# Kernel tuning notes

Hardware: AMD Instinct MI355X
Metric: run time of the kernel (lower is better)

The kernel has to match this reference:

```python
import jax, jax.numpy as jnp
import numpy as np

EPS = 1e-5
RS = 2                 # trilinear sampling points per bin per dim (fixed sampling_ratio)
OUT_SIZE = (4, 7, 7)   # (T_out, H_out, W_out)


def hswish(x):
    return x * jnp.clip(x + 3.0, 0.0, 6.0) / 6.0


def bn3d(x, g, b, m, v):
    # eval-mode BatchNorm3d over channel dim 1 of [N,C,T,H,W]
    s = g * jax.lax.rsqrt(v + EPS)
    return x * s[None, :, None, None, None] + (b - m * s)[None, :, None, None, None]


def conv3d(x, w, stride=1, pad=0, groups=1):
    return jax.lax.conv_general_dilated(
        x, w, window_strides=(stride,) * 3, padding=[(pad, pad)] * 3,
        dimension_numbers=('NCDHW', 'OIDHW', 'NCDHW'), feature_group_count=groups)


def roi_align_3d(feat, start, end):
    # feat: [N,C,T,H,W]; start/end: [N,3] in (x, y, t) order (one ROI per sample)
    N, C, T, H, W = feat.shape
    Pt, Ph, Pw = OUT_SIZE

    def coords(s, e, P):
        size = jnp.maximum(e - s, 1.0)
        # flattened sample j = bin*RS + i -> position s + (j+0.5)/RS * bin_size
        offs = (jnp.arange(P * RS, dtype=feat.dtype) + 0.5) / RS
        return s[:, None] + offs[None, :] * (size / P)[:, None]  # [N, P*RS]

    cx = coords(start[:, 0], end[:, 0], Pw)
    cy = coords(start[:, 1], end[:, 1], Ph)
    ct = coords(start[:, 2], end[:, 2], Pt)

    def lin(v, c, L):
        # linear interpolation of v along its last axis at continuous coords c
        c = jnp.clip(c, 0.0, L - 1.0)
        lo = jnp.floor(c).astype(jnp.int32)
        hi = jnp.minimum(lo + 1, L - 1)
        w = c - lo.astype(c.dtype)
        return v[..., lo] * (1.0 - w) + v[..., hi] * w

    def one(f, tt, ty, tx):
        f = lin(f, tx, W)                   # [C,T,H,Sw]
        f = jnp.moveaxis(f, 2, -1)          # [C,T,Sw,H]
        f = lin(f, ty, H)                   # [C,T,Sw,Sh]
        f = jnp.moveaxis(f, 1, -1)          # [C,Sw,Sh,T]
        f = lin(f, tt, T)                   # [C,Sw,Sh,St]
        f = jnp.transpose(f, (0, 3, 2, 1))  # [C,St,Sh,Sw]
        f = f.reshape(f.shape[0], Pt, RS, Ph, RS, Pw, RS)
        return f.mean(axis=(2, 4, 6))       # average sample points per bin

    return jax.vmap(one)(feat, ct, cy, cx)  # [N,C,Pt,Ph,Pw]


def setup_inputs():
    key = jax.random.key(0)
    ks = jax.random.split(key, 9)
    N, Cin, T, H, W = 64, 256, 8, 16, 16
    Cr = 128

    def bn_params(k, c):
        k1, k2, k3, k4 = jax.random.split(k, 4)
        g = jax.random.uniform(k1, (c,), minval=0.5, maxval=1.5)
        b = 0.1 * jax.random.normal(k2, (c,))
        m = 0.1 * jax.random.normal(k3, (c,))
        v = jax.random.uniform(k4, (c,), minval=0.5, maxval=1.5)
        return g, b, m, v

    x = jax.random.normal(ks[0], (N, Cin, T, H, W), jnp.float32)
    w1 = jax.random.normal(ks[1], (Cr, Cin, 1, 1, 1)) / np.float32(np.sqrt(Cin))
    wdw = jax.random.normal(ks[2], (Cr, 1, 3, 3, 3)) / np.float32(np.sqrt(27))
    w2 = jax.random.normal(ks[3], (Cr, Cr, 1, 1, 1)) / np.float32(np.sqrt(Cr))
    w3 = jax.random.normal(ks[4], (6, Cr, 1, 1, 1)) / np.float32(np.sqrt(Cr))
    g1, b1, m1, v1 = bn_params(ks[5], Cr)
    g2, b2, m2, v2 = bn_params(ks[6], Cr)
    g3, b3, m3, v3 = bn_params(ks[7], Cr)
    g4, b4, m4, v4 = bn_params(ks[8], 6)
    return dict(x=x, w1=w1, g1=g1, b1=b1, m1=m1, v1=v1,
                wdw=wdw, g2=g2, b2=b2, m2=m2, v2=v2,
                w2=w2, g3=g3, b3=b3, m3=m3, v3=v3,
                w3=w3, g4=g4, b4=b4, m4=m4, v4=v4)


def reference(x, w1, g1, b1, m1, v1, wdw, g2, b2, m2, v2,
              w2, g3, b3, m3, v3, w3, g4, b4, m4, v4):
    N, C, T, H, W = x.shape
    h = hswish(bn3d(conv3d(x, w1), g1, b1, m1, v1))
    h = hswish(bn3d(conv3d(h, wdw, stride=2, pad=1, groups=wdw.shape[0]), g2, b2, m2, v2))
    h = hswish(bn3d(conv3d(h, w2), g3, b3, m3, v3))
    # AvgPool3d with kernel == reduced feature size -> global spatial-temporal mean
    h = jnp.mean(h, axis=(2, 3, 4), keepdims=True)
    logits = bn3d(conv3d(h, w3), g4, b4, m4, v4).reshape(N, 6)
    lim = jax.nn.sigmoid(logits)   # eval path (gumbel only in training)
    scales = jnp.array([W, H, T], dtype=x.dtype)      # (x, y, t) order
    start = 0.5 * lim[:, :3] * scales
    end = (1.0 - 0.5 * lim[:, 3:]) * scales
    return roi_align_3d(x, start, end)
```

## Files before the change

### kernel.cpp

```cpp
#include <hip/hip_runtime.h>
#include <math.h>

#define N_BATCH 64
#define CIN 256
#define CR 128
#define T_IN 8
#define H_IN 16
#define W_IN 16
#define S1 2048
#define T2 4
#define H2 8
#define W2 8
#define S2 256
#define PT 4
#define PH 7
#define PW 7
#define EPSB 1e-5f

typedef __attribute__((ext_vector_type(8))) short bf16x8;
typedef __attribute__((ext_vector_type(4))) float f32x4;
typedef __attribute__((ext_vector_type(4))) unsigned int u32x4;
typedef __attribute__((ext_vector_type(8))) unsigned short ushort8;

__device__ __forceinline__ float hswish(float y) {
    float c = fminf(fmaxf(y + 3.0f, 0.0f), 6.0f);
    return y * c * (1.0f / 6.0f);
}

__device__ __forceinline__ unsigned int fbits(float x) {
    return __float_as_uint(x);
}

__device__ __forceinline__ unsigned int pkbf16(float lo, float hi) {
    return ((fbits(lo) + 0x8000u) >> 16) | ((fbits(hi) + 0x8000u) & 0xFFFF0000u);
}

__global__ __launch_bounds__(256) void wsplit_kernel(
    const float* __restrict__ w1, unsigned short* __restrict__ whi,
    unsigned short* __restrict__ wlo, float* __restrict__ pp)
{
    int i = blockIdx.x * 256 + threadIdx.x;
    int co = i >> 8;
    int k  = i & 255;
    float x = w1[i];
    unsigned int bx = fbits(x);
    unsigned int h = (bx + 0x8000u) & 0xFFFF0000u;
    float r = x - __uint_as_float(h);
    int flat = ((((co >> 4) * 8 + (k >> 5)) * 4 + ((k >> 3) & 3)) * 16 + (co & 15)) * 8 + (k & 7);
    whi[flat] = (unsigned short)(h >> 16);
    wlo[flat] = (unsigned short)((fbits(r) + 0x8000u) >> 16);
    pp[i] = 0.0f;
}

#define BFIDX(g, h, e, ln) (((((g) * 2 + (h)) * 2 + (e)) * 16 + (ln)) * 4)

__global__ __launch_bounds__(256, 5) void conv1_mfma_kernel(
    const float* __restrict__ x,
    const unsigned short* __restrict__ whi, const unsigned short* __restrict__ wlo,
    const float* __restrict__ g, const float* __restrict__ b,
    const float* __restrict__ m, const float* __restrict__ v,
    unsigned short* __restrict__ h1b)
{
    __shared__ unsigned int Bf[2][1024];

    int blk = blockIdx.x;
    int n  = blk >> 5;
    int s0 = (blk & 31) << 6;
    int tid = threadIdx.x;
    int wave = tid >> 6;
    int lane = tid & 63;
    int gl   = lane >> 4;
    int ln16 = lane & 15;
    int hw   = wave & 1;
    int wcoG = (wave >> 1) * 4;

    int sg = tid >> 6;
    int sc = tid & 63;
    int sh = sc >> 5;
    int se = sc & 1;
    int sl = (sc & 31) >> 1;
    int wslot = BFIDX(sg, sh, se, sl);
    const float* xg = x + (size_t)n * CIN * S1 + s0 + sc;

    f32x4 acc[4][2];
    #pragma unroll
    for (int i = 0; i < 4; i++) {
        acc[i][0] = (f32x4){0.f, 0.f, 0.f, 0.f};
        acc[i][1] = (f32x4){0.f, 0.f, 0.f, 0.f};
    }

    {
        float val[8];
        #pragma unroll
        for (int j = 0; j < 8; j++)
            val[j] = xg[(size_t)(sg * 8 + j) * S1];
        u32x4 w;
        #pragma unroll
        for (int p = 0; p < 4; p++)
            w[p] = pkbf16(val[2 * p], val[2 * p + 1]);
        *reinterpret_cast<u32x4*>(&Bf[0][wslot]) = w;
    }
    __syncthreads();

    #pragma unroll
    for (int ks = 0; ks < 8; ks++) {
        float val[8];
        if (ks < 7) {
            #pragma unroll
            for (int j = 0; j < 8; j++)
                val[j] = xg[(size_t)((ks + 1) * 32 + sg * 8 + j) * S1];
        }
        union { u32x4 u; bf16x8 bv; } B0, B1;
        B0.u = *reinterpret_cast<const u32x4*>(&Bf[ks & 1][BFIDX(gl, hw, 0, ln16)]);
        B1.u = *reinterpret_cast<const u32x4*>(&Bf[ks & 1][BFIDX(gl, hw, 1, ln16)]);
        {
            bf16x8 Ah[4];
            #pragma unroll
            for (int fc = 0; fc < 4; fc++) {
                int off = ((((wcoG + fc) * 8 + ks) * 4 + gl) * 16 + ln16) * 8;
                Ah[fc] = *reinterpret_cast<const bf16x8*>(whi + off);
            }
            #pragma unroll
            for (int fc = 0; fc < 4; fc++) {
                acc[fc][0] = __builtin_amdgcn_mfma_f32_16x16x32_bf16(Ah[fc], B0.bv, acc[fc][0], 0, 0, 0);
                acc[fc][1] = __builtin_amdgcn_mfma_f32_16x16x32_bf16(Ah[fc], B1.bv, acc[fc][1], 0, 0, 0);
            }
        }
        {
            bf16x8 Al[4];
            #pragma unroll
            for (int fc = 0; fc < 4; fc++) {
                int off = ((((wcoG + fc) * 8 + ks) * 4 + gl) * 16 + ln16) * 8;
                Al[fc] = *reinterpret_cast<const bf16x8*>(wlo + off);
            }
            #pragma unroll
            for (int fc = 0; fc < 4; fc++) {
                acc[fc][0] = __builtin_amdgcn_mfma_f32_16x16x32_bf16(Al[fc], B0.bv, acc[fc][0], 0, 0, 0);
                acc[fc][1] = __builtin_amdgcn_mfma_f32_16x16x32_bf16(Al[fc], B1.bv, acc[fc][1], 0, 0, 0);
            }
        }
        if (ks < 7) {
            u32x4 w;
            #pragma unroll
            for (int p = 0; p < 4; p++)
                w[p] = pkbf16(val[2 * p], val[2 * p + 1]);
            *reinterpret_cast<u32x4*>(&Bf[(ks + 1) & 1][wslot]) = w;
            __syncthreads();
        }
    }

    #pragma unroll
    for (int fc = 0; fc < 4; fc++)
        #pragma unroll
        for (int reg = 0; reg < 4; reg++) {
            int co = (wcoG + fc) * 16 + gl * 4 + reg;
            float sc_ = g[co] * rsqrtf(v[co] + EPSB);
            float tt = fmaf(-m[co], sc_, b[co]);
            float y0 = hswish(fmaf(acc[fc][0][reg], sc_, tt));
            float y1 = hswish(fmaf(acc[fc][1][reg], sc_, tt));
            unsigned int pk = pkbf16(y0, y1);
            *reinterpret_cast<unsigned int*>(
                h1b + ((size_t)n * CR + co) * S1 + s0 + hw * 32 + ln16 * 2) = pk;
        }
}

__global__ __launch_bounds__(256) void dwconv_kernel(
    const unsigned short* __restrict__ h1b, const float* __restrict__ wdw,
    const float* __restrict__ g, const float* __restrict__ b,
    const float* __restrict__ m, const float* __restrict__ v,
    float* __restrict__ h2)
{
    __shared__ float s[T_IN][H_IN][W_IN];
    __shared__ float wl[27];
    int blk = blockIdx.x;
    int n = blk >> 7;
    int c = blk & 127;
    int tid = threadIdx.x;
    const unsigned short* in = h1b + ((size_t)n * CR + c) * S1;

    {
        int e = tid * 8;
        ushort8 u = *reinterpret_cast<const ushort8*>(in + e);
        float* sp = &s[0][0][0] + e;
        #pragma unroll
        for (int i = 0; i < 8; i++)
            sp[i] = __uint_as_float((unsigned int)(unsigned short)u[i] << 16);
    }
    if (tid < 27) wl[tid] = wdw[c * 27 + tid];
    __syncthreads();

    int wo = tid & 7;
    int ho = (tid >> 3) & 7;
    int to = tid >> 6;
    float acc = 0.0f;
    #pragma unroll
    for (int dt = 0; dt < 3; dt++) {
        int ti = 2 * to - 1 + dt;
        if (ti < 0 || ti >= T_IN) continue;
        #pragma unroll
        for (int dh = 0; dh < 3; dh++) {
            int hi = 2 * ho - 1 + dh;
            if (hi < 0 || hi >= H_IN) continue;
            #pragma unroll
            for (int dw = 0; dw < 3; dw++) {
                int wi = 2 * wo - 1 + dw;
                if (wi < 0 || wi >= W_IN) continue;
                acc = fmaf(wl[(dt * 3 + dh) * 3 + dw], s[ti][hi][wi], acc);
            }
        }
    }
    float sc = g[c] * rsqrtf(v[c] + EPSB);
    float y  = fmaf(acc, sc, fmaf(-m[c], sc, b[c]));
    h2[((size_t)n * CR + c) * S2 + tid] = hswish(y);
}

#define KC 16
__global__ __launch_bounds__(256) void conv2_kernel(
    const float* __restrict__ h2, const float* __restrict__ w2,
    const float* __restrict__ g, const float* __restrict__ b,
    const float* __restrict__ m, const float* __restrict__ v,
    float* __restrict__ pp)
{
    __shared__ float Xs[KC][64];
    __shared__ float Ws[KC][CR + 4];

    int blk = blockIdx.x;
    int n  = blk >> 2;
    int sq = blk & 3;
    int s0 = sq << 6;
    int tid = threadIdx.x;
    int tco = tid >> 3;
    int ts  = tid & 7;
    const float* xn = h2 + (size_t)n * CR * S2;

    float acc[4][8];
    #pragma unroll
    for (int i = 0; i < 4; i++)
        #pragma unroll
        for (int j = 0; j < 8; j++) acc[i][j] = 0.0f;

    for (int k0 = 0; k0 < CR; k0 += KC) {
        {
            int e  = tid * 4;
            int kk = e >> 6;
            int ss = e & 63;
            float4 xv = *reinterpret_cast<const float4*>(xn + (size_t)(k0 + kk) * S2 + s0 + ss);
            *reinterpret_cast<float4*>(&Xs[kk][ss]) = xv;
        }
        #pragma unroll
        for (int r = 0; r < 8; r++) {
            int e  = tid + r * 256;
            int co = e >> 4;
            int kk = e & 15;
            Ws[kk][co] = w2[co * CR + k0 + kk];
        }
        __syncthreads();
        #pragma unroll
        for (int kk = 0; kk < KC; kk++) {
            float a[4], bb[8];
            #pragma unroll
            for (int r = 0; r < 4; r++) a[r] = Ws[kk][tco * 4 + r];
            #pragma unroll
            for (int q = 0; q < 8; q++) bb[q] = Xs[kk][ts * 8 + q];
            #pragma unroll
            for (int r = 0; r < 4; r++)
                #pragma unroll
                for (int q = 0; q < 8; q++)
                    acc[r][q] = fmaf(a[r], bb[q], acc[r][q]);
        }
        __syncthreads();
    }

    #pragma unroll
    for (int r = 0; r < 4; r++) {
        int co = tco * 4 + r;
        float sc = g[co] * rsqrtf(v[co] + EPSB);
        float tt = fmaf(-m[co], sc, b[co]);
        float psum = 0.0f;
        #pragma unroll
        for (int q = 0; q < 8; q++)
            psum += hswish(fmaf(acc[r][q], sc, tt));
        #pragma unroll
        for (int off = 4; off > 0; off >>= 1)
            psum += __shfl_down(psum, off, 8);
        if (ts == 0)
            pp[((size_t)n * CR + co) * 4 + sq] = psum;
    }
}

__global__ __launch_bounds__(128) void head_kernel(
    const float* __restrict__ pp, const float* __restrict__ w3,
    const float* __restrict__ g, const float* __restrict__ b,
    const float* __restrict__ m, const float* __restrict__ v,
    float* __restrict__ boxes)
{
    __shared__ float red[2];
    int n = blockIdx.x;
    int c = threadIdx.x;
    int wave = c >> 6, lane = c & 63;
    const float* p = pp + ((size_t)n * CR + c) * 4;
    float pc = (p[0] + p[1] + p[2] + p[3]) * (1.0f / 256.0f);

    for (int j = 0; j < 6; j++) {
        float t = w3[j * CR + c] * pc;
        #pragma unroll
        for (int off = 32; off > 0; off >>= 1)
            t += __shfl_down(t, off, 64);
        if (lane == 0) red[wave] = t;
        __syncthreads();
        if (c == 0) {
            float acc = red[0] + red[1];
            float sc = g[j] * rsqrtf(v[j] + EPSB);
            float logit = fmaf(acc, sc, fmaf(-m[j], sc, b[j]));
            float lim = 1.0f / (1.0f + expf(-logit));
            float scale = ((j % 3) == 2) ? 8.0f : 16.0f;
            float val = (j < 3) ? 0.5f * lim * scale : (1.0f - 0.5f * lim) * scale;
            boxes[n * 6 + j] = val;
        }
        __syncthreads();
    }
}

__global__ __launch_bounds__(256) void roi_kernel(
    const float* __restrict__ x, const float* __restrict__ boxes,
    float* __restrict__ out)
{
    __shared__ float s[T_IN][H_IN][W_IN];
    __shared__ float box[6];
    int blk = blockIdx.x;
    int n = blk >> 8;
    int c = blk & 255;
    int tid = threadIdx.x;
    const float* in = x + ((size_t)n * CIN + c) * S1;
    #pragma unroll
    for (int r = 0; r < 2; r++) {
        int e = (tid + r * 256) * 4;
        *reinterpret_cast<float4*>(&s[0][0][0] + e) =
            *reinterpret_cast<const float4*>(in + e);
    }
    if (tid < 6) box[tid] = boxes[n * 6 + tid];
    __syncthreads();

    if (tid < PT * PH * PW) {
        int pw = tid % 7;
        int ph = (tid / 7) % 7;
        int pt = tid / 49;
        float sx = box[0], sy = box[1], st = box[2];
        float bszx = fmaxf(box[3] - sx, 1.0f) * (1.0f / PW);
        float bszy = fmaxf(box[4] - sy, 1.0f) * (1.0f / PH);
        float bszt = fmaxf(box[5] - st, 1.0f) * (1.0f / PT);

        float acc = 0.0f;
        #pragma unroll
        for (int it = 0; it < 2; it++) {
            float tc = st + ((float)(pt * 2 + it) + 0.5f) * 0.5f * bszt;
            tc = fminf(fmaxf(tc, 0.0f), (float)(T_IN - 1));
            int tlo = (int)floorf(tc);
            int thi = min(tlo + 1, T_IN - 1);
            float tw = tc - (float)tlo;
            #pragma unroll
            for (int iy = 0; iy < 2; iy++) {
                float yc = sy + ((float)(ph * 2 + iy) + 0.5f) * 0.5f * bszy;
                yc = fminf(fmaxf(yc, 0.0f), (float)(H_IN - 1));
                int ylo = (int)floorf(yc);
                int yhi = min(ylo + 1, H_IN - 1);
                float yw = yc - (float)ylo;
                #pragma unroll
                for (int ix = 0; ix < 2; ix++) {
                    float xc = sx + ((float)(pw * 2 + ix) + 0.5f) * 0.5f * bszx;
                    xc = fminf(fmaxf(xc, 0.0f), (float)(W_IN - 1));
                    int xlo = (int)floorf(xc);
                    int xhi = min(xlo + 1, W_IN - 1);
                    float xw = xc - (float)xlo;

                    float v00 = s[tlo][ylo][xlo] * (1.0f - xw) + s[tlo][ylo][xhi] * xw;
                    float v01 = s[tlo][yhi][xlo] * (1.0f - xw) + s[tlo][yhi][xhi] * xw;
                    float v10 = s[thi][ylo][xlo] * (1.0f - xw) + s[thi][ylo][xhi] * xw;
                    float v11 = s[thi][yhi][xlo] * (1.0f - xw) + s[thi][yhi][xhi] * xw;
                    float v0 = v00 * (1.0f - yw) + v01 * yw;
                    float v1 = v10 * (1.0f - yw) + v11 * yw;
                    acc += v0 * (1.0f - tw) + v1 * tw;
                }
            }
        }
        out[(((size_t)(n * CIN + c) * PT + pt) * PH + ph) * PW + pw] = acc * 0.125f;
    }
}

extern "C" void kernel_launch(void* const* d_in, const int* in_sizes, int n_in,
                              void* d_out, int out_size, void* d_ws, size_t ws_size,
                              hipStream_t stream) {
    const float* x   = (const float*)d_in[0];
    const float* w1  = (const float*)d_in[1];
    const float* g1  = (const float*)d_in[2];
    const float* b1  = (const float*)d_in[3];
    const float* m1  = (const float*)d_in[4];
    const float* v1  = (const float*)d_in[5];
    const float* wdw = (const float*)d_in[6];
    const float* g2  = (const float*)d_in[7];
    const float* b2  = (const float*)d_in[8];
    const float* m2  = (const float*)d_in[9];
    const float* v2  = (const float*)d_in[10];
    const float* w2  = (const float*)d_in[11];
    const float* g3  = (const float*)d_in[12];
    const float* b3  = (const float*)d_in[13];
    const float* m3  = (const float*)d_in[14];
    const float* v3  = (const float*)d_in[15];
    const float* w3  = (const float*)d_in[16];
    const float* g4  = (const float*)d_in[17];
    const float* b4  = (const float*)d_in[18];
    const float* m4  = (const float*)d_in[19];
    const float* v4  = (const float*)d_in[20];

    float* ws = (float*)d_ws;
    float* h1     = ws;
    float* h2     = h1 + (size_t)N_BATCH * CR * S1;
    float* h3     = h2 + (size_t)N_BATCH * CR * S2;
    float* pp     = h3 + (size_t)N_BATCH * CR * S2;
    float* boxes  = pp + (size_t)N_BATCH * CR * 4;
    unsigned short* h1b = (unsigned short*)h1;
    unsigned short* whi = (unsigned short*)h3;
    unsigned short* wlo = whi + CR * CIN;

    wsplit_kernel<<<dim3(128), dim3(256), 0, stream>>>(w1, whi, wlo, pp);
    conv1_mfma_kernel<<<dim3(2048), dim3(256), 0, stream>>>(x, whi, wlo, g1, b1, m1, v1, h1b);
    dwconv_kernel<<<dim3(N_BATCH * CR), dim3(256), 0, stream>>>(h1b, wdw, g2, b2, m2, v2, h2);
    conv2_kernel<<<dim3(256), dim3(256), 0, stream>>>(h2, w2, g3, b3, m3, v3, pp);
    head_kernel<<<dim3(N_BATCH), dim3(128), 0, stream>>>(pp, w3, g4, b4, m4, v4, boxes);
    roi_kernel<<<dim3(N_BATCH * CIN), dim3(256), 0, stream>>>(x, boxes, (float*)d_out);
}
```

Baseline: 124.2 us.

## Retile conv1 MFMA to 256-column blocks with direct global-to-LDS async loads

The 1x1 conv1 kernel now processes 256 spatial columns per block with 512 threads, so each weight fragment feeds four MFMA column tiles instead of two. Input activations are copied as fp32 straight into XOR-swizzled LDS with global_load_lds, replacing the register staging and bf16 pack before the LDS store. The bf16 conversion moves to after the LDS read, which frees VGPRs during the prefetch and lets the async copy overlap the MFMAs. In exchange the kernel uses 64 KB of LDS per block and launches a quarter as many blocks, which may lower occupancy and load balance.

```diff
diff --git a/kernel.cpp b/kernel.cpp
--- a/kernel.cpp
+++ b/kernel.cpp
@@ -52,115 +52,119 @@
     pp[i] = 0.0f;
 }
 
-#define BFIDX(g, h, e, ln) (((((g) * 2 + (h)) * 2 + (e)) * 16 + (ln)) * 4)
-
-__global__ __launch_bounds__(256, 5) void conv1_mfma_kernel(
+__global__ __launch_bounds__(512, 4) void conv1_mfma_kernel(
     const float* __restrict__ x,
     const unsigned short* __restrict__ whi, const unsigned short* __restrict__ wlo,
     const float* __restrict__ g, const float* __restrict__ b,
     const float* __restrict__ m, const float* __restrict__ v,
     unsigned short* __restrict__ h1b)
 {
-    __shared__ unsigned int Bf[2][1024];
+    __shared__ float X[2][32 * 256];
 
     int blk = blockIdx.x;
-    int n  = blk >> 5;
-    int s0 = (blk & 31) << 6;
+    int n  = blk >> 3;
+    int s0 = (blk & 7) << 8;
     int tid = threadIdx.x;
-    int wave = tid >> 6;
+    int w    = tid >> 6;
     int lane = tid & 63;
     int gl   = lane >> 4;
     int ln16 = lane & 15;
-    int hw   = wave & 1;
-    int wcoG = (wave >> 1) * 4;
-
-    int sg = tid >> 6;
-    int sc = tid & 63;
-    int sh = sc >> 5;
-    int se = sc & 1;
-    int sl = (sc & 31) >> 1;
-    int wslot = BFIDX(sg, sh, se, sl);
-    const float* xg = x + (size_t)n * CIN * S1 + s0 + sc;
-
-    f32x4 acc[4][2];
+    int wcoH = w >> 2;
+    int wq   = w & 3;
+
+    const float* xn = x + (size_t)n * CIN * S1 + s0;
+
+    f32x4 acc[4][4];
+    #pragma unroll
+    for (int i = 0; i < 4; i++)
+        #pragma unroll
+        for (int j = 0; j < 4; j++)
+            acc[i][j] = (f32x4){0.f, 0.f, 0.f, 0.f};
+
+    int qbase = (wq * 16 + ln16) ^ (gl << 1);
+
     #pragma unroll
     for (int i = 0; i < 4; i++) {
-        acc[i][0] = (f32x4){0.f, 0.f, 0.f, 0.f};
-        acc[i][1] = (f32x4){0.f, 0.f, 0.f, 0.f};
-    }
-
-    {
-        float val[8];
-        #pragma unroll
-        for (int j = 0; j < 8; j++)
-            val[j] = xg[(size_t)(sg * 8 + j) * S1];
-        u32x4 w;
-        #pragma unroll
-        for (int p = 0; p < 4; p++)
-            w[p] = pkbf16(val[2 * p], val[2 * p + 1]);
-        *reinterpret_cast<u32x4*>(&Bf[0][wslot]) = w;
+        int r = w * 4 + i;
+        int C = (r & 7) ^ (((r >> 3) & 3) << 1);
+        const float* src = xn + (size_t)r * S1 + ((lane ^ C) << 2);
+        __builtin_amdgcn_global_load_lds(
+            (const __attribute__((address_space(1))) unsigned int*)src,
+            (__attribute__((address_space(3))) unsigned int*)&X[0][r * 256],
+            16, 0, 0);
     }
     __syncthreads();
 
     #pragma unroll
     for (int ks = 0; ks < 8; ks++) {
-        float val[8];
+        const int cur = ks & 1;
+        bf16x8 Ah[4];
+        #pragma unroll
+        for (int fc = 0; fc < 4; fc++) {
+            int off = ((((wcoH * 4 + fc) * 8 + ks) * 4 + gl) * 16 + ln16) * 8;
+            Ah[fc] = *reinterpret_cast<const bf16x8*>(whi + off);
+        }
         if (ks < 7) {
             #pragma unroll
-            for (int j = 0; j < 8; j++)
-                val[j] = xg[(size_t)((ks + 1) * 32 + sg * 8 + j) * S1];
-        }
-        union { u32x4 u; bf16x8 bv; } B0, B1;
-        B0.u = *reinterpret_cast<const u32x4*>(&Bf[ks & 1][BFIDX(gl, hw, 0, ln16)]);
-        B1.u = *reinterpret_cast<const u32x4*>(&Bf[ks & 1][BFIDX(gl, hw, 1, ln16)]);
-        {
-            bf16x8 Ah[4];
-            #pragma unroll
-            for (int fc = 0; fc < 4; fc++) {
-                int off = ((((wcoG + fc) * 8 + ks) * 4 + gl) * 16 + ln16) * 8;
-                Ah[fc] = *reinterpret_cast<const bf16x8*>(whi + off);
+            for (int i = 0; i < 4; i++) {
+                int r = w * 4 + i;
+                int C = (r & 7) ^ (((r >> 3) & 3) << 1);
+                const float* src = xn + (size_t)((ks + 1) * 32 + r) * S1 + ((lane ^ C) << 2);
+                __builtin_amdgcn_global_load_lds(
+                    (const __attribute__((address_space(1))) unsigned int*)src,
+                    (__attribute__((address_space(3))) unsigned int*)&X[cur ^ 1][r * 256],
+                    16, 0, 0);
             }
-            #pragma unroll
-            for (int fc = 0; fc < 4; fc++) {
-                acc[fc][0] = __builtin_amdgcn_mfma_f32_16x16x32_bf16(Ah[fc], B0.bv, acc[fc][0], 0, 0, 0);
-                acc[fc][1] = __builtin_amdgcn_mfma_f32_16x16x32_bf16(Ah[fc], B1.bv, acc[fc][1], 0, 0, 0);
-            }
-        }
-        {
-            bf16x8 Al[4];
-            #pragma unroll
-            for (int fc = 0; fc < 4; fc++) {
-                int off = ((((wcoG + fc) * 8 + ks) * 4 + gl) * 16 + ln16) * 8;
-                Al[fc] = *reinterpret_cast<const bf16x8*>(wlo + off);
-            }
-            #pragma unroll
-            for (int fc = 0; fc < 4; fc++) {
-                acc[fc][0] = __builtin_amdgcn_mfma_f32_16x16x32_bf16(Al[fc], B0.bv, acc[fc][0], 0, 0, 0);
-                acc[fc][1] = __builtin_amdgcn_mfma_f32_16x16x32_bf16(Al[fc], B1.bv, acc[fc][1], 0, 0, 0);
-            }
-        }
-        if (ks < 7) {
-            u32x4 w;
+        }
+        f32x4 rd[8];
+        #pragma unroll
+        for (int j = 0; j < 8; j++) {
+            int off = ((gl * 8 + j) << 8) + ((qbase ^ j) << 2);
+            rd[j] = *reinterpret_cast<const f32x4*>(&X[cur][off]);
+        }
+        union { u32x4 u; bf16x8 bv; } Bp[4];
+        #pragma unroll
+        for (int fs = 0; fs < 4; fs++)
             #pragma unroll
             for (int p = 0; p < 4; p++)
-                w[p] = pkbf16(val[2 * p], val[2 * p + 1]);
-            *reinterpret_cast<u32x4*>(&Bf[(ks + 1) & 1][wslot]) = w;
-            __syncthreads();
-        }
+                Bp[fs].u[p] = pkbf16(rd[2 * p][fs], rd[2 * p + 1][fs]);
+        #pragma unroll
+        for (int fc = 0; fc < 4; fc++)
+            #pragma unroll
+            for (int fs = 0; fs < 4; fs++)
+                acc[fc][fs] = __builtin_amdgcn_mfma_f32_16x16x32_bf16(
+                    Ah[fc], Bp[fs].bv, acc[fc][fs], 0, 0, 0);
+        bf16x8 Al[4];
+        #pragma unroll
+        for (int fc = 0; fc < 4; fc++) {
+            int off = ((((wcoH * 4 + fc) * 8 + ks) * 4 + gl) * 16 + ln16) * 8;
+            Al[fc] = *reinterpret_cast<const bf16x8*>(wlo + off);
+        }
+        #pragma unroll
+        for (int fc = 0; fc < 4; fc++)
+            #pragma unroll
+            for (int fs = 0; fs < 4; fs++)
+                acc[fc][fs] = __builtin_amdgcn_mfma_f32_16x16x32_bf16(
+                    Al[fc], Bp[fs].bv, acc[fc][fs], 0, 0, 0);
+        if (ks < 7) __syncthreads();
     }
 
     #pragma unroll
     for (int fc = 0; fc < 4; fc++)
         #pragma unroll
         for (int reg = 0; reg < 4; reg++) {
-            int co = (wcoG + fc) * 16 + gl * 4 + reg;
+            int co = wcoH * 64 + fc * 16 + gl * 4 + reg;
             float sc_ = g[co] * rsqrtf(v[co] + EPSB);
             float tt = fmaf(-m[co], sc_, b[co]);
             float y0 = hswish(fmaf(acc[fc][0][reg], sc_, tt));
             float y1 = hswish(fmaf(acc[fc][1][reg], sc_, tt));
-            unsigned int pk = pkbf16(y0, y1);
-            *reinterpret_cast<unsigned int*>(
-                h1b + ((size_t)n * CR + co) * S1 + s0 + hw * 32 + ln16 * 2) = pk;
+            float y2 = hswish(fmaf(acc[fc][2][reg], sc_, tt));
+            float y3 = hswish(fmaf(acc[fc][3][reg], sc_, tt));
+            uint2 pk;
+            pk.x = pkbf16(y0, y1);
+            pk.y = pkbf16(y2, y3);
+            *reinterpret_cast<uint2*>(
+                h1b + ((size_t)n * CR + co) * S1 + s0 + wq * 64 + ln16 * 4) = pk;
         }
 }
 
@@ -423,7 +427,7 @@
     unsigned short* wlo = whi + CR * CIN;
 
     wsplit_kernel<<<dim3(128), dim3(256), 0, stream>>>(w1, whi, wlo, pp);
-    conv1_mfma_kernel<<<dim3(2048), dim3(256), 0, stream>>>(x, whi, wlo, g1, b1, m1, v1, h1b);
+    conv1_mfma_kernel<<<dim3(512), dim3(512), 0, stream>>>(x, whi, wlo, g1, b1, m1, v1, h1b);
     dwconv_kernel<<<dim3(N_BATCH * CR), dim3(256), 0, stream>>>(h1b, wdw, g2, b2, m2, v2, h2);
     conv2_kernel<<<dim3(256), dim3(256), 0, stream>>>(h2, w2, g3, b3, m3, v3, pp);
     head_kernel<<<dim3(N_BATCH), dim3(128), 0, stream>>>(pp, w3, g4, b4, m4, v4, boxes);
```

Result: slower. 144.2 us (+16.2%).

## Deepen conv1 input prefetch to two stages and hoist weight loads

Applied to the files above, without the earlier changes.

The pointwise conv1 MFMA loop now keeps a three-slot register ring of input values, so global loads run two K-steps ahead instead of one. The bf16 pack and LDS store for the next step now happen before the MFMAs rather than after, and both hi/lo weight fragments are loaded together at the top of each step. The aim is to hide global-load latency behind more MFMA work and give the scheduler freedom to interleave. The cost is higher register pressure (24 extra floats plus all 8 A fragments live at once), which could lower occupancy.

```diff
diff --git a/kernel.cpp b/kernel.cpp
--- a/kernel.cpp
+++ b/kernel.cpp
@@ -89,64 +89,57 @@
         acc[i][1] = (f32x4){0.f, 0.f, 0.f, 0.f};
     }
 
+    float val[3][8];
+    #pragma unroll
+    for (int j = 0; j < 8; j++)
+        val[0][j] = xg[(size_t)(sg * 8 + j) * S1];
+    #pragma unroll
+    for (int j = 0; j < 8; j++)
+        val[1][j] = xg[(size_t)(32 + sg * 8 + j) * S1];
     {
-        float val[8];
-        #pragma unroll
-        for (int j = 0; j < 8; j++)
-            val[j] = xg[(size_t)(sg * 8 + j) * S1];
-        u32x4 w;
+        u32x4 wv;
         #pragma unroll
         for (int p = 0; p < 4; p++)
-            w[p] = pkbf16(val[2 * p], val[2 * p + 1]);
-        *reinterpret_cast<u32x4*>(&Bf[0][wslot]) = w;
+            wv[p] = pkbf16(val[0][2 * p], val[0][2 * p + 1]);
+        *reinterpret_cast<u32x4*>(&Bf[0][wslot]) = wv;
     }
     __syncthreads();
 
     #pragma unroll
     for (int ks = 0; ks < 8; ks++) {
-        float val[8];
+        bf16x8 Ah[4], Al[4];
+        #pragma unroll
+        for (int fc = 0; fc < 4; fc++) {
+            int off = ((((wcoG + fc) * 8 + ks) * 4 + gl) * 16 + ln16) * 8;
+            Ah[fc] = *reinterpret_cast<const bf16x8*>(whi + off);
+            Al[fc] = *reinterpret_cast<const bf16x8*>(wlo + off);
+        }
+        if (ks < 6) {
+            #pragma unroll
+            for (int j = 0; j < 8; j++)
+                val[(ks + 2) % 3][j] = xg[(size_t)((ks + 2) * 32 + sg * 8 + j) * S1];
+        }
         if (ks < 7) {
-            #pragma unroll
-            for (int j = 0; j < 8; j++)
-                val[j] = xg[(size_t)((ks + 1) * 32 + sg * 8 + j) * S1];
+            u32x4 wv;
+            #pragma unroll
+            for (int p = 0; p < 4; p++)
+                wv[p] = pkbf16(val[(ks + 1) % 3][2 * p], val[(ks + 1) % 3][2 * p + 1]);
+            *reinterpret_cast<u32x4*>(&Bf[(ks + 1) & 1][wslot]) = wv;
         }
         union { u32x4 u; bf16x8 bv; } B0, B1;
         B0.u = *reinterpret_cast<const u32x4*>(&Bf[ks & 1][BFIDX(gl, hw, 0, ln16)]);
         B1.u = *reinterpret_cast<const u32x4*>(&Bf[ks & 1][BFIDX(gl, hw, 1, ln16)]);
-        {
-            bf16x8 Ah[4];
-            #pragma unroll
-            for (int fc = 0; fc < 4; fc++) {
-                int off = ((((wcoG + fc) * 8 + ks) * 4 + gl) * 16 + ln16) * 8;
-                Ah[fc] = *reinterpret_cast<const bf16x8*>(whi + off);
-            }
-            #pragma unroll
-            for (int fc = 0; fc < 4; fc++) {
-                acc[fc][0] = __builtin_amdgcn_mfma_f32_16x16x32_bf16(Ah[fc], B0.bv, acc[fc][0], 0, 0, 0);
-                acc[fc][1] = __builtin_amdgcn_mfma_f32_16x16x32_bf16(Ah[fc], B1.bv, acc[fc][1], 0, 0, 0);
-            }
-        }
-        {
-            bf16x8 Al[4];
-            #pragma unroll
-            for (int fc = 0; fc < 4; fc++) {
-                int off = ((((wcoG + fc) * 8 + ks) * 4 + gl) * 16 + ln16) * 8;
-                Al[fc] = *reinterpret_cast<const bf16x8*>(wlo + off);
-            }
-            #pragma unroll
-            for (int fc = 0; fc < 4; fc++) {
-                acc[fc][0] = __builtin_amdgcn_mfma_f32_16x16x32_bf16(Al[fc], B0.bv, acc[fc][0], 0, 0, 0);
-                acc[fc][1] = __builtin_amdgcn_mfma_f32_16x16x32_bf16(Al[fc], B1.bv, acc[fc][1], 0, 0, 0);
-            }
-        }
-        if (ks < 7) {
-            u32x4 w;
-            #pragma unroll
-            for (int p = 0; p < 4; p++)
-                w[p] = pkbf16(val[2 * p], val[2 * p + 1]);
-            *reinterpret_cast<u32x4*>(&Bf[(ks + 1) & 1][wslot]) = w;
-            __syncthreads();
-        }
+        #pragma unroll
+        for (int fc = 0; fc < 4; fc++) {
+            acc[fc][0] = __builtin_amdgcn_mfma_f32_16x16x32_bf16(Ah[fc], B0.bv, acc[fc][0], 0, 0, 0);
+            acc[fc][1] = __builtin_amdgcn_mfma_f32_16x16x32_bf16(Ah[fc], B1.bv, acc[fc][1], 0, 0, 0);
+        }
+        #pragma unroll
+        for (int fc = 0; fc < 4; fc++) {
+            acc[fc][0] = __builtin_amdgcn_mfma_f32_16x16x32_bf16(Al[fc], B0.bv, acc[fc][0], 0, 0, 0);
+            acc[fc][1] = __builtin_amdgcn_mfma_f32_16x16x32_bf16(Al[fc], B1.bv, acc[fc][1], 0, 0, 0);
+        }
+        if (ks < 7) __syncthreads();
     }
 
     #pragma unroll
```

Result: no change. 125.3 us (+0.9%).
